# Kernel tuning notes

Measured on AMD Instinct MI355X. Metric: run time of the kernel, lower is better.

Reference implementation:

```python
import jax, jax.numpy as jnp
import numpy as np

N, DIM, H, HD, RD, QLR, OLR, G = 64, 4096, 32, 192, 64, 1536, 512, 8
BS, MAXB, L, NBLK, TOPK, EPS = 64, 64, 4096, 4096, 1024, 1e-6
SLOTS = NBLK * BS
SCALE = HD ** -0.5
NEG = -1e30


def _rms(x, w, eps=EPS):
    return x * jax.lax.rsqrt(jnp.mean(x * x, -1, keepdims=True) + eps) * w


def _rope(x, pos):
    # x: [..., RD]; pos broadcastable to x.shape[:-1]; interleaved pairs
    half = RD // 2
    inv = 1.0 / (10000.0 ** (jnp.arange(half, dtype=jnp.float32) * 2.0 / RD))
    ang = pos[..., None].astype(jnp.float32) * inv  # [..., half]
    c, s = jnp.cos(ang), jnp.sin(ang)
    xr = x.reshape(x.shape[:-1] + (half, 2))
    x0, x1 = xr[..., 0], xr[..., 1]
    return jnp.stack([x0 * c - x1 * s, x0 * s + x1 * c], -1).reshape(x.shape)


def setup_inputs() -> dict:
    key = jax.random.key(0)
    ks = jax.random.split(key, 12)
    block_tables = jax.random.permutation(ks[0], jnp.arange(N * MAXB, dtype=jnp.int32)).reshape(N, MAXB)
    context_lens = jax.random.randint(ks[1], (N,), 1, L, dtype=jnp.int32)
    last = context_lens - 1
    slot_mapping = (block_tables[jnp.arange(N), last // BS] * BS + last % BS).astype(jnp.int32)
    def w(k, shape, fan_in):
        return jax.random.normal(k, shape, jnp.float32) * (fan_in ** -0.5)
    return {
        'x': jax.random.normal(ks[2], (N, DIM), jnp.float32),
        'kv_cache': jax.random.normal(ks[3], (SLOTS, HD), jnp.float32),
        'block_tables': block_tables,
        'context_lens': context_lens,
        'slot_mapping': slot_mapping,
        'wq_a_w': w(ks[4], (QLR, DIM), DIM),
        'q_norm_w': jnp.ones((QLR,), jnp.float32),
        'wq_b_w': w(ks[5], (H * HD, QLR), QLR),
        'wkv_w': w(ks[6], (HD, DIM), DIM),
        'kv_norm_w': jnp.ones((HD,), jnp.float32),
        'wo_a_w': w(ks[7], (G, OLR, H * HD // G), H * HD // G),
        'wo_b_w': w(ks[8], (DIM, G * OLR), G * OLR),
        'attn_sink': jax.random.normal(ks[9], (H,), jnp.float32),
    }


def reference(x, kv_cache, block_tables, context_lens, slot_mapping,
              wq_a_w, q_norm_w, wq_b_w, wkv_w, kv_norm_w,
              wo_a_w, wo_b_w, attn_sink):
    pos = (context_lens - 1).astype(jnp.float32)  # [N] query positions
    # --- queries: LoRA down-proj -> RMSNorm -> up-proj -> heads ---
    q = _rms(x @ wq_a_w.T, q_norm_w) @ wq_b_w.T            # [N, H*HD]
    q = q.reshape(N, H, HD)
    q = jnp.concatenate([q[..., :HD - RD], _rope(q[..., HD - RD:], pos[:, None])], -1)
    # --- new KV latent + paged write (slot_mapping scatter) ---
    kv = _rms(x @ wkv_w.T, kv_norm_w)                       # [N, HD]
    kv = jnp.concatenate([kv[:, :HD - RD], _rope(kv[:, HD - RD:], pos)], -1)
    cache = kv_cache.at[slot_mapping].set(kv)
    # --- paged gather into dense per-request view [N, L, HD] ---
    ar = jnp.arange(L)
    slot = block_tables[:, ar // BS] * BS + ar % BS         # [N, L]
    valid = ar[None, :] < context_lens[:, None]             # [N, L]
    kv_dense = cache[jnp.where(valid, slot, 0)]
    kv_dense = jnp.where(valid[..., None], kv_dense, 0.0)
    # --- sparse top-k attention with sink logit ---
    logits = jnp.einsum('nhd,nld->nhl', q, kv_dense) * SCALE
    logits = jnp.where(valid[:, None, :], logits, NEG)
    vals, idx = jax.lax.top_k(logits, TOPK)                 # [N, H, K]
    sink = attn_sink[None, :, None]                         # [1, H, 1]
    m = jnp.maximum(jnp.max(vals, -1, keepdims=True), sink)
    e = jnp.exp(vals - m)
    denom = jnp.sum(e, -1, keepdims=True) + jnp.exp(sink - m)
    p = e / denom                                           # [N, H, K]
    probs = jnp.put_along_axis(jnp.zeros_like(logits), idx, p, axis=-1, inplace=False)
    o = jnp.einsum('nhl,nld->nhd', probs, kv_dense)         # [N, H, HD]
    # --- grouped LoRA output projection ---
    og = o.reshape(N, G, H * HD // G)
    lat = jnp.einsum('ngi,goi->ngo', og, wo_a_w).reshape(N, G * OLR)
    return lat @ wo_b_w.T                                   # [N, DIM]
```

## Files before the change

### kernel.cpp

```cpp
#include <hip/hip_runtime.h>
#include <hip/hip_bf16.h>

static constexpr float EPS_   = 1e-6f;
static constexpr float SCALE_ = 0.07216878364870323f;
static constexpr float LOG2_1E4_OVER_32 = 13.287712379549449f / 32.0f;

static constexpr long OFF_QLAT = 0;
static constexpr long OFF_Q    = OFF_QLAT + 64L * 1536;
static constexpr long OFF_KVR  = OFF_Q    + 64L * 6144;
static constexpr long OFF_O    = OFF_KVR  + 64L * 192;
static constexpr long OFF_LAT  = OFF_O    + 64L * 6144;
static constexpr long ZERO_F   = OFF_LAT  + 64L * 4096;
static constexpr long OFF_SELM = ZERO_F;
static constexpr long OFF_SELI = OFF_SELM + 2048;
static constexpr long OFF_SELT = OFF_SELI + 2048;
static constexpr long OFF_LOG  = OFF_SELT + 2048;

typedef __attribute__((ext_vector_type(8))) short bf16x8;
typedef __attribute__((ext_vector_type(4))) float f32x4;

__device__ __forceinline__ unsigned fkey(float f) {
    unsigned u = __float_as_uint(f);
    return (u & 0x80000000u) ? ~u : (u | 0x80000000u);
}
__device__ __forceinline__ float kval(unsigned k) {
    unsigned u = (k & 0x80000000u) ? (k ^ 0x80000000u) : ~k;
    return __uint_as_float(u);
}
__device__ __forceinline__ unsigned short f2bf(float f) {
    __hip_bfloat16 h = __float2bfloat16(f);
    return *reinterpret_cast<unsigned short*>(&h);
}
__device__ __forceinline__ bf16x8 pack8(float4 v0, float4 v1) {
    bf16x8 s;
    s[0] = (short)f2bf(v0.x); s[1] = (short)f2bf(v0.y);
    s[2] = (short)f2bf(v0.z); s[3] = (short)f2bf(v0.w);
    s[4] = (short)f2bf(v1.x); s[5] = (short)f2bf(v1.y);
    s[6] = (short)f2bf(v1.z); s[7] = (short)f2bf(v1.w);
    return s;
}

template <int TN>
__global__ __launch_bounds__(256) void gemm_mfma(
    const float* __restrict__ Xb, const float* __restrict__ Wb,
    float* __restrict__ Cb, int K, int ldX, int ldC, int kslice,
    long sXz, long sWz, long sCz)
{
    const float* X = Xb + (long)blockIdx.z * sXz;
    const float* W = Wb + (long)blockIdx.z * sWz;
    float*       C = Cb + (long)blockIdx.z * sCz;
    const int col0 = blockIdx.x * TN;
    const int k0   = blockIdx.y * kslice;

    __shared__ unsigned short Xs[64 * 64];
    __shared__ unsigned short Ws[TN * 64];

    const int t = threadIdx.x;
    const int w = t >> 6, lane = t & 63;
    const int m16 = lane & 15, qd = lane >> 4;
    constexpr int NT = TN / 64;

    f32x4 acc[4][NT];
#pragma unroll
    for (int mt = 0; mt < 4; ++mt)
#pragma unroll
        for (int nt = 0; nt < NT; ++nt) acc[mt][nt] = (f32x4){0.f, 0.f, 0.f, 0.f};

    for (int kt = k0; kt < k0 + kslice; kt += 64) {
#pragma unroll
        for (int i = 0; i < 2; ++i) {
            int idx = t + i * 256;
            int r = idx >> 3, u = idx & 7;
            const float* p = X + (long)r * ldX + kt + u * 8;
            float4 v0 = *(const float4*)p, v1 = *(const float4*)(p + 4);
            *(bf16x8*)(Xs + r * 64 + (u ^ (r & 7)) * 8) = pack8(v0, v1);
        }
#pragma unroll
        for (int i = 0; i < TN / 32; ++i) {
            int idx = t + i * 256;
            int r = idx >> 3, u = idx & 7;
            const float* p = W + (long)(col0 + r) * K + kt + u * 8;
            float4 v0 = *(const float4*)p, v1 = *(const float4*)(p + 4);
            *(bf16x8*)(Ws + r * 64 + (u ^ (r & 7)) * 8) = pack8(v0, v1);
        }
        __syncthreads();
#pragma unroll
        for (int ks = 0; ks < 2; ++ks) {
            int u = ks * 4 + qd;
            bf16x8 a[4], b[NT];
#pragma unroll
            for (int mt = 0; mt < 4; ++mt) {
                int row = mt * 16 + m16;
                a[mt] = *(const bf16x8*)(Xs + row * 64 + (u ^ (row & 7)) * 8);
            }
#pragma unroll
            for (int nt = 0; nt < NT; ++nt) {
                int row = (w * NT + nt) * 16 + m16;
                b[nt] = *(const bf16x8*)(Ws + row * 64 + (u ^ (row & 7)) * 8);
            }
#pragma unroll
            for (int mt = 0; mt < 4; ++mt)
#pragma unroll
                for (int nt = 0; nt < NT; ++nt)
                    acc[mt][nt] = __builtin_amdgcn_mfma_f32_16x16x32_bf16(a[mt], b[nt], acc[mt][nt], 0, 0, 0);
        }
        __syncthreads();
    }
#pragma unroll
    for (int mt = 0; mt < 4; ++mt)
#pragma unroll
        for (int nt = 0; nt < NT; ++nt) {
            int col = col0 + (w * NT + nt) * 16 + m16;
#pragma unroll
            for (int r = 0; r < 4; ++r) {
                int row = mt * 16 + qd * 4 + r;
                atomicAdd(&C[(long)row * ldC + col], acc[mt][nt][r]);
            }
        }
}

__global__ __launch_bounds__(256) void rms_rows(
    float* __restrict__ x, const float* __restrict__ w, int len)
{
    __shared__ float fred[4];
    float* row = x + (long)blockIdx.x * len;
    int t = threadIdx.x;
    float ss = 0.f;
    for (int l = t; l < len; l += 256) { float v = row[l]; ss += v * v; }
#pragma unroll
    for (int off = 32; off; off >>= 1) ss += __shfl_xor(ss, off, 64);
    if ((t & 63) == 0) fred[t >> 6] = ss;
    __syncthreads();
    ss = fred[0] + fred[1] + fred[2] + fred[3];
    float scale = rsqrtf(ss / (float)len + EPS_);
    for (int l = t; l < len; l += 256) row[l] = row[l] * scale * w[l];
}

__global__ __launch_bounds__(256) void rope_q(float* __restrict__ q,
                                              const int* __restrict__ cl)
{
    int n = blockIdx.x;
    float pos = (float)(cl[n] - 1);
    int t = threadIdx.x;
#pragma unroll
    for (int i = 0; i < 4; ++i) {
        int f = t + i * 256;
        int h = f >> 5, r = f & 31;
        float inv = exp2f(-(float)r * LOG2_1E4_OVER_32);
        float ang = pos * inv;
        float sn, cs;
        sincosf(ang, &sn, &cs);
        float* p = q + (long)n * 6144 + h * 192 + 128 + 2 * r;
        float x0 = p[0], x1 = p[1];
        p[0] = x0 * cs - x1 * sn;
        p[1] = x0 * sn + x1 * cs;
    }
}

__global__ __launch_bounds__(256) void kv_post(
    const float* __restrict__ kvr, const float* __restrict__ wnorm,
    const int* __restrict__ cl, const int* __restrict__ smap,
    float* __restrict__ kvcache)
{
    __shared__ float s[192];
    __shared__ float fred[4];
    int n = blockIdx.x, t = threadIdx.x;
    float v = (t < 192) ? kvr[(long)n * 192 + t] : 0.f;
    float ss = v * v;
#pragma unroll
    for (int off = 32; off; off >>= 1) ss += __shfl_xor(ss, off, 64);
    if ((t & 63) == 0) fred[t >> 6] = ss;
    __syncthreads();
    ss = fred[0] + fred[1] + fred[2] + fred[3];
    float scale = rsqrtf(ss / 192.f + EPS_);
    if (t < 192) s[t] = v * scale * wnorm[t];
    __syncthreads();
    if (t < 32) {
        float pos = (float)(cl[n] - 1);
        float inv = exp2f(-(float)t * LOG2_1E4_OVER_32);
        float ang = pos * inv;
        float sn, cs;
        sincosf(ang, &sn, &cs);
        float x0 = s[128 + 2 * t], x1 = s[128 + 2 * t + 1];
        s[128 + 2 * t]     = x0 * cs - x1 * sn;
        s[128 + 2 * t + 1] = x0 * sn + x1 * cs;
    }
    __syncthreads();
    if (t < 192) kvcache[(long)smap[n] * 192 + t] = s[t];
}

__global__ __launch_bounds__(256) void attn_logits_mfma(
    const float* __restrict__ q, const float* __restrict__ kvc,
    const int* __restrict__ bt, const int* __restrict__ cl,
    float* __restrict__ logits)
{
    const int n = blockIdx.y, base = blockIdx.x * 128;
    const int ctx = cl[n];
    if (base >= ctx) return;

    __shared__ unsigned short qs[32 * 192];
    __shared__ unsigned short kvs[128 * 192];
    const int t = threadIdx.x;

#pragma unroll
    for (int i = 0; i < 3; ++i) {
        int idx = t + i * 256;
        int h = idx / 24, u = idx - h * 24;
        const float* p = q + (long)n * 6144 + h * 192 + u * 8;
        float4 v0 = *(const float4*)p, v1 = *(const float4*)(p + 4);
        *(bf16x8*)(qs + h * 192 + (u ^ (h & 7)) * 8) = pack8(v0, v1);
    }
#pragma unroll
    for (int i = 0; i < 12; ++i) {
        int idx = t + i * 256;
        int l = idx / 24, u = idx - l * 24;
        int gl = min(base + l, ctx - 1);
        int slot = bt[n * 64 + (gl >> 6)] * 64 + (gl & 63);
        const float* p = kvc + (long)slot * 192 + u * 8;
        float4 v0 = *(const float4*)p, v1 = *(const float4*)(p + 4);
        *(bf16x8*)(kvs + l * 192 + (u ^ (l & 7)) * 8) = pack8(v0, v1);
    }
    __syncthreads();

    const int w = t >> 6, lane = t & 63;
    const int m16 = lane & 15, qd = lane >> 4;

    f32x4 acc[2][2];
#pragma unroll
    for (int mt = 0; mt < 2; ++mt)
#pragma unroll
        for (int nt = 0; nt < 2; ++nt) acc[mt][nt] = (f32x4){0.f, 0.f, 0.f, 0.f};

#pragma unroll
    for (int ks = 0; ks < 6; ++ks) {
        int u = ks * 4 + qd;
        bf16x8 a[2], b[2];
#pragma unroll
        for (int mt = 0; mt < 2; ++mt) {
            int row = mt * 16 + m16;
            a[mt] = *(const bf16x8*)(qs + row * 192 + (u ^ (row & 7)) * 8);
        }
#pragma unroll
        for (int nt = 0; nt < 2; ++nt) {
            int row = (2 * w + nt) * 16 + m16;
            b[nt] = *(const bf16x8*)(kvs + row * 192 + (u ^ (row & 7)) * 8);
        }
#pragma unroll
        for (int mt = 0; mt < 2; ++mt)
#pragma unroll
            for (int nt = 0; nt < 2; ++nt)
                acc[mt][nt] = __builtin_amdgcn_mfma_f32_16x16x32_bf16(a[mt], b[nt], acc[mt][nt], 0, 0, 0);
    }
#pragma unroll
    for (int mt = 0; mt < 2; ++mt)
#pragma unroll
        for (int nt = 0; nt < 2; ++nt) {
            int l = base + (2 * w + nt) * 16 + m16;
#pragma unroll
            for (int r = 0; r < 4; ++r) {
                int h = mt * 16 + qd * 4 + r;
                logits[((long)(n * 32 + h) << 12) + l] = acc[mt][nt][r] * SCALE_;
            }
        }
}

__global__ __launch_bounds__(256) void select_topk(
    const float* __restrict__ logits, const int* __restrict__ cl,
    const float* __restrict__ sink, float* __restrict__ selm,
    float* __restrict__ seli, unsigned* __restrict__ selt)
{
    int nh = blockIdx.x, n = nh >> 5, h = nh & 31;
    int ctx = cl[n];
    const float* row = logits + ((long)nh << 12);

    __shared__ unsigned keys[4096];
    __shared__ int hist[256];
    __shared__ float fred[4];
    __shared__ unsigned s_pref;
    __shared__ int s_R;

    int t = threadIdx.x;
    float mx = -3.0e38f;
    for (int l = t; l < ctx; l += 256) {
        float v = row[l];
        keys[l] = fkey(v);
        mx = fmaxf(mx, v);
    }
#pragma unroll
    for (int off = 32; off; off >>= 1) mx = fmaxf(mx, __shfl_xor(mx, off, 64));
    if ((t & 63) == 0) fred[t >> 6] = mx;
    __syncthreads();
    mx = fmaxf(fmaxf(fred[0], fred[1]), fmaxf(fred[2], fred[3]));

    unsigned tau = 0;
    if (ctx > 1024) {
        unsigned pref = 0;
        int R = 1024;
        for (int round = 3; round >= 0; --round) {
            int sh = round * 8;
            hist[t] = 0;
            __syncthreads();
            for (int l = t; l < ctx; l += 256) {
                unsigned k = keys[l];
                bool match = (round == 3) || ((k >> (sh + 8)) == (pref >> (sh + 8)));
                if (match) atomicAdd(&hist[(k >> sh) & 255], 1);
            }
            __syncthreads();
            int cum = 0;
            for (int b = t + 1; b < 256; ++b) cum += hist[b];
            if (cum < R && cum + hist[t] >= R) {
                s_pref = pref | ((unsigned)t << sh);
                s_R = R - cum;
            }
            __syncthreads();
            pref = s_pref;
            R = s_R;
            __syncthreads();
        }
        tau = pref;
    }

    float m = fmaxf(mx, sink[h]);
    float part = 0.f;
    for (int l = t; l < ctx; l += 256) {
        unsigned k = keys[l];
        if (k >= tau) part += __expf(kval(k) - m);
    }
#pragma unroll
    for (int off = 32; off; off >>= 1) part += __shfl_xor(part, off, 64);
    __syncthreads();
    if ((t & 63) == 0) fred[t >> 6] = part;
    __syncthreads();
    if (t == 0) {
        float denom = fred[0] + fred[1] + fred[2] + fred[3] + __expf(sink[h] - m);
        selm[nh] = m;
        seli[nh] = 1.0f / denom;
        selt[nh] = tau;
    }
}

__global__ __launch_bounds__(256) void attn_wsum_mfma(
    const float* __restrict__ logits, const float* __restrict__ kvc,
    const int* __restrict__ bt, const int* __restrict__ cl,
    const float* __restrict__ selm, const float* __restrict__ seli,
    const unsigned* __restrict__ selt, float* __restrict__ o)
{
    const int n = blockIdx.y, base = blockIdx.x * 128;
    const int ctx = cl[n];
    if (base >= ctx) return;
    const int vcount = min(128, ctx - base);

    __shared__ unsigned short ps[32 * 128];
    __shared__ unsigned short kvt[192 * 128];
    const int t = threadIdx.x;

#pragma unroll
    for (int i = 0; i < 2; ++i) {
        int idx = t + i * 256;
        int h = idx >> 4, u = idx & 15;
        int nh = n * 32 + h;
        float m = selm[nh], inv = seli[nh];
        unsigned tau = selt[nh];
        const float* lp = logits + ((long)nh << 12) + base + u * 8;
        float4 v0 = *(const float4*)lp, v1 = *(const float4*)(lp + 4);
        float vv[8] = {v0.x, v0.y, v0.z, v0.w, v1.x, v1.y, v1.z, v1.w};
        bf16x8 s;
#pragma unroll
        for (int j = 0; j < 8; ++j) {
            int ll = u * 8 + j;
            float p = 0.f;
            if (ll < vcount && fkey(vv[j]) >= tau) p = __expf(vv[j] - m) * inv;
            s[j] = (short)f2bf(p);
        }
        *(bf16x8*)(ps + h * 128 + (u ^ (h & 7)) * 8) = s;
    }
#pragma unroll
    for (int i = 0; i < 24; ++i) {
        int f = t + i * 256;
        int l = f & 127, d4 = f >> 7;
        int gl = min(base + l, ctx - 1);
        int slot = bt[n * 64 + (gl >> 6)] * 64 + (gl & 63);
        float4 v = *(const float4*)(kvc + (long)slot * 192 + d4 * 4);
        float vv[4] = {v.x, v.y, v.z, v.w};
#pragma unroll
        for (int e = 0; e < 4; ++e) {
            int d = d4 * 4 + e;
            int scol = (l & 7) | ((((l >> 3) ^ (d & 7)) & 15) << 3);
            kvt[d * 128 + scol] = f2bf(vv[e]);
        }
    }
    __syncthreads();

    const int w = t >> 6, lane = t & 63;
    const int m16 = lane & 15, qd = lane >> 4;

    f32x4 acc[2][3];
#pragma unroll
    for (int mt = 0; mt < 2; ++mt)
#pragma unroll
        for (int nt = 0; nt < 3; ++nt) acc[mt][nt] = (f32x4){0.f, 0.f, 0.f, 0.f};

#pragma unroll
    for (int ks = 0; ks < 4; ++ks) {
        int u = ks * 4 + qd;
        bf16x8 a[2], b[3];
#pragma unroll
        for (int mt = 0; mt < 2; ++mt) {
            int row = mt * 16 + m16;
            a[mt] = *(const bf16x8*)(ps + row * 128 + (u ^ (row & 7)) * 8);
        }
#pragma unroll
        for (int nt = 0; nt < 3; ++nt) {
            int row = (3 * w + nt) * 16 + m16;
            b[nt] = *(const bf16x8*)(kvt + row * 128 + (u ^ (row & 7)) * 8);
        }
#pragma unroll
        for (int mt = 0; mt < 2; ++mt)
#pragma unroll
            for (int nt = 0; nt < 3; ++nt)
                acc[mt][nt] = __builtin_amdgcn_mfma_f32_16x16x32_bf16(a[mt], b[nt], acc[mt][nt], 0, 0, 0);
    }
#pragma unroll
    for (int mt = 0; mt < 2; ++mt)
#pragma unroll
        for (int nt = 0; nt < 3; ++nt) {
            int d = (3 * w + nt) * 16 + m16;
#pragma unroll
            for (int r = 0; r < 4; ++r) {
                int h = mt * 16 + qd * 4 + r;
                atomicAdd(&o[(long)n * 6144 + h * 192 + d], acc[mt][nt][r]);
            }
        }
}

extern "C" void kernel_launch(void* const* d_in, const int* in_sizes, int n_in,
                              void* d_out, int out_size, void* d_ws, size_t ws_size,
                              hipStream_t stream)
{
    const float* x    = (const float*)d_in[0];
    float*       kvc  = (float*)d_in[1];
    const int*   bt   = (const int*)d_in[2];
    const int*   cl   = (const int*)d_in[3];
    const int*   smap = (const int*)d_in[4];
    const float* wqa  = (const float*)d_in[5];
    const float* qnw  = (const float*)d_in[6];
    const float* wqb  = (const float*)d_in[7];
    const float* wkv  = (const float*)d_in[8];
    const float* kvnw = (const float*)d_in[9];
    const float* woa  = (const float*)d_in[10];
    const float* wob  = (const float*)d_in[11];
    const float* sink = (const float*)d_in[12];
    float* ws  = (float*)d_ws;
    float* out = (float*)d_out;

    hipMemsetAsync(ws, 0, (size_t)ZERO_F * sizeof(float), stream);
    hipMemsetAsync(out, 0, (size_t)out_size * sizeof(float), stream);

    gemm_mfma<128><<<dim3(12, 16, 1), 256, 0, stream>>>(x, wqa, ws + OFF_QLAT,
                                                        4096, 4096, 1536, 256, 0, 0, 0);
    rms_rows<<<64, 256, 0, stream>>>(ws + OFF_QLAT, qnw, 1536);
    gemm_mfma<128><<<dim3(48, 6, 1), 256, 0, stream>>>(ws + OFF_QLAT, wqb, ws + OFF_Q,
                                                       1536, 1536, 6144, 256, 0, 0, 0);
    rope_q<<<64, 256, 0, stream>>>(ws + OFF_Q, cl);
    gemm_mfma<64><<<dim3(3, 32, 1), 256, 0, stream>>>(x, wkv, ws + OFF_KVR,
                                                      4096, 4096, 192, 128, 0, 0, 0);
    kv_post<<<64, 256, 0, stream>>>(ws + OFF_KVR, kvnw, cl, smap, kvc);
    attn_logits_mfma<<<dim3(32, 64), 256, 0, stream>>>(ws + OFF_Q, kvc, bt, cl,
                                                       ws + OFF_LOG);
    select_topk<<<2048, 256, 0, stream>>>(ws + OFF_LOG, cl, sink,
                                          ws + OFF_SELM, ws + OFF_SELI,
                                          (unsigned*)(ws + OFF_SELT));
    attn_wsum_mfma<<<dim3(32, 64), 256, 0, stream>>>(ws + OFF_LOG, kvc, bt, cl,
                                                     ws + OFF_SELM, ws + OFF_SELI,
                                                     (unsigned*)(ws + OFF_SELT),
                                                     ws + OFF_O);
    gemm_mfma<128><<<dim3(4, 3, 8), 256, 0, stream>>>(ws + OFF_O, woa, ws + OFF_LAT,
                                                      768, 6144, 4096, 256,
                                                      768, 512L * 768, 512);
    gemm_mfma<128><<<dim3(32, 8, 1), 256, 0, stream>>>(ws + OFF_LAT, wob, out,
                                                       4096, 4096, 4096, 512, 0, 0, 0);
}
```

Baseline: 541.2 us.

## Aggregate histogram atomics, scan-based radix bucket search, and two chunks per attention block

The top-k select kernel now builds its first radix histogram during the key-load pass, using wave-aggregated atomics, which removes one full pass over the keys. It also replaces the serial per-thread suffix sum over bins with a wave shuffle scan plus cross-wave sums. The logits and weighted-sum attention kernels each process two 128-token chunks per block, halving the grid. In wsum this halves the number of fp32 atomic flushes into the output and hoists the per-head selection parameters out of the loop. The trade-off is fewer blocks in flight and longer serial work per block, since each chunk is loaded behind a barrier with no overlap.

Measured after the change: 549.1 us. About the same (+1.5%).

```diff
diff --git a/kernel.cpp b/kernel.cpp
--- a/kernel.cpp
+++ b/kernel.cpp
@@ -38,6 +38,19 @@
     s[4] = (short)f2bf(v1.x); s[5] = (short)f2bf(v1.y);
     s[6] = (short)f2bf(v1.z); s[7] = (short)f2bf(v1.w);
     return s;
+}
+
+__device__ __forceinline__ void hist_add_agg(int* hist, unsigned bin, bool pred) {
+    const int lane = (int)(threadIdx.x & 63);
+    while (__any(pred)) {
+        unsigned long long act = __ballot(pred);
+        int leader = __ffsll((unsigned long long)act) - 1;
+        unsigned lbin = (unsigned)__shfl((int)bin, leader, 64);
+        bool mine = pred && (bin == lbin);
+        unsigned long long grp = __ballot(mine);
+        if (lane == leader) atomicAdd(&hist[lbin], (int)__popcll(grp));
+        if (mine) pred = false;
+    }
 }
 
 template <int TN>
@@ -194,13 +207,15 @@
     const int* __restrict__ bt, const int* __restrict__ cl,
     float* __restrict__ logits)
 {
-    const int n = blockIdx.y, base = blockIdx.x * 128;
+    const int n = blockIdx.y, sbase = blockIdx.x * 256;
     const int ctx = cl[n];
-    if (base >= ctx) return;
+    if (sbase >= ctx) return;
 
     __shared__ unsigned short qs[32 * 192];
     __shared__ unsigned short kvs[128 * 192];
     const int t = threadIdx.x;
+    const int w = t >> 6, lane = t & 63;
+    const int m16 = lane & 15, qd = lane >> 4;
 
 #pragma unroll
     for (int i = 0; i < 3; ++i) {
@@ -210,58 +225,62 @@
         float4 v0 = *(const float4*)p, v1 = *(const float4*)(p + 4);
         *(bf16x8*)(qs + h * 192 + (u ^ (h & 7)) * 8) = pack8(v0, v1);
     }
-#pragma unroll
-    for (int i = 0; i < 12; ++i) {
-        int idx = t + i * 256;
-        int l = idx / 24, u = idx - l * 24;
-        int gl = min(base + l, ctx - 1);
-        int slot = bt[n * 64 + (gl >> 6)] * 64 + (gl & 63);
-        const float* p = kvc + (long)slot * 192 + u * 8;
-        float4 v0 = *(const float4*)p, v1 = *(const float4*)(p + 4);
-        *(bf16x8*)(kvs + l * 192 + (u ^ (l & 7)) * 8) = pack8(v0, v1);
-    }
-    __syncthreads();
-
-    const int w = t >> 6, lane = t & 63;
-    const int m16 = lane & 15, qd = lane >> 4;
-
-    f32x4 acc[2][2];
-#pragma unroll
-    for (int mt = 0; mt < 2; ++mt)
-#pragma unroll
-        for (int nt = 0; nt < 2; ++nt) acc[mt][nt] = (f32x4){0.f, 0.f, 0.f, 0.f};
-
-#pragma unroll
-    for (int ks = 0; ks < 6; ++ks) {
-        int u = ks * 4 + qd;
-        bf16x8 a[2], b[2];
-#pragma unroll
-        for (int mt = 0; mt < 2; ++mt) {
-            int row = mt * 16 + m16;
-            a[mt] = *(const bf16x8*)(qs + row * 192 + (u ^ (row & 7)) * 8);
-        }
-#pragma unroll
-        for (int nt = 0; nt < 2; ++nt) {
-            int row = (2 * w + nt) * 16 + m16;
-            b[nt] = *(const bf16x8*)(kvs + row * 192 + (u ^ (row & 7)) * 8);
-        }
+
+    for (int c = 0; c < 2; ++c) {
+        const int base = sbase + c * 128;
+        if (base >= ctx) break;
+
+#pragma unroll
+        for (int i = 0; i < 12; ++i) {
+            int idx = t + i * 256;
+            int l = idx / 24, u = idx - l * 24;
+            int gl = min(base + l, ctx - 1);
+            int slot = bt[n * 64 + (gl >> 6)] * 64 + (gl & 63);
+            const float* p = kvc + (long)slot * 192 + u * 8;
+            float4 v0 = *(const float4*)p, v1 = *(const float4*)(p + 4);
+            *(bf16x8*)(kvs + l * 192 + (u ^ (l & 7)) * 8) = pack8(v0, v1);
+        }
+        __syncthreads();
+
+        f32x4 acc[2][2];
 #pragma unroll
         for (int mt = 0; mt < 2; ++mt)
 #pragma unroll
-            for (int nt = 0; nt < 2; ++nt)
-                acc[mt][nt] = __builtin_amdgcn_mfma_f32_16x16x32_bf16(a[mt], b[nt], acc[mt][nt], 0, 0, 0);
-    }
-#pragma unroll
-    for (int mt = 0; mt < 2; ++mt)
-#pragma unroll
-        for (int nt = 0; nt < 2; ++nt) {
-            int l = base + (2 * w + nt) * 16 + m16;
-#pragma unroll
-            for (int r = 0; r < 4; ++r) {
-                int h = mt * 16 + qd * 4 + r;
-                logits[((long)(n * 32 + h) << 12) + l] = acc[mt][nt][r] * SCALE_;
-            }
-        }
+            for (int nt = 0; nt < 2; ++nt) acc[mt][nt] = (f32x4){0.f, 0.f, 0.f, 0.f};
+
+#pragma unroll
+        for (int ks = 0; ks < 6; ++ks) {
+            int u = ks * 4 + qd;
+            bf16x8 a[2], b[2];
+#pragma unroll
+            for (int mt = 0; mt < 2; ++mt) {
+                int row = mt * 16 + m16;
+                a[mt] = *(const bf16x8*)(qs + row * 192 + (u ^ (row & 7)) * 8);
+            }
+#pragma unroll
+            for (int nt = 0; nt < 2; ++nt) {
+                int row = (2 * w + nt) * 16 + m16;
+                b[nt] = *(const bf16x8*)(kvs + row * 192 + (u ^ (row & 7)) * 8);
+            }
+#pragma unroll
+            for (int mt = 0; mt < 2; ++mt)
+#pragma unroll
+                for (int nt = 0; nt < 2; ++nt)
+                    acc[mt][nt] = __builtin_amdgcn_mfma_f32_16x16x32_bf16(a[mt], b[nt], acc[mt][nt], 0, 0, 0);
+        }
+#pragma unroll
+        for (int mt = 0; mt < 2; ++mt)
+#pragma unroll
+            for (int nt = 0; nt < 2; ++nt) {
+                int l = base + (2 * w + nt) * 16 + m16;
+#pragma unroll
+                for (int r = 0; r < 4; ++r) {
+                    int h = mt * 16 + qd * 4 + r;
+                    logits[((long)(n * 32 + h) << 12) + l] = acc[mt][nt][r] * SCALE_;
+                }
+            }
+        __syncthreads();
+    }
 }
 
 __global__ __launch_bounds__(256) void select_topk(
@@ -276,39 +295,70 @@
     __shared__ unsigned keys[4096];
     __shared__ int hist[256];
     __shared__ float fred[4];
+    __shared__ int wsumi[4];
     __shared__ unsigned s_pref;
     __shared__ int s_R;
 
     int t = threadIdx.x;
+    int lane = t & 63, wv = t >> 6;
+    bool need_radix = (ctx > 1024);
+
+    hist[t] = 0;
+    __syncthreads();
+
     float mx = -3.0e38f;
-    for (int l = t; l < ctx; l += 256) {
-        float v = row[l];
-        keys[l] = fkey(v);
-        mx = fmaxf(mx, v);
+    for (int l0 = 0; l0 < ctx; l0 += 256) {
+        int l = l0 + t;
+        bool valid = l < ctx;
+        unsigned k = 0;
+        if (valid) {
+            float v = row[l];
+            k = fkey(v);
+            keys[l] = k;
+            mx = fmaxf(mx, v);
+        }
+        if (need_radix) hist_add_agg(hist, k >> 24, valid);
     }
 #pragma unroll
     for (int off = 32; off; off >>= 1) mx = fmaxf(mx, __shfl_xor(mx, off, 64));
-    if ((t & 63) == 0) fred[t >> 6] = mx;
+    if (lane == 0) fred[wv] = mx;
     __syncthreads();
     mx = fmaxf(fmaxf(fred[0], fred[1]), fmaxf(fred[2], fred[3]));
 
     unsigned tau = 0;
-    if (ctx > 1024) {
+    if (need_radix) {
         unsigned pref = 0;
         int R = 1024;
         for (int round = 3; round >= 0; --round) {
             int sh = round * 8;
-            hist[t] = 0;
+            if (round < 3) {
+                hist[t] = 0;
+                __syncthreads();
+                for (int l0 = 0; l0 < ctx; l0 += 256) {
+                    int l = l0 + t;
+                    if (l < ctx) {
+                        unsigned k = keys[l];
+                        if ((k >> (sh + 8)) == (pref >> (sh + 8)))
+                            atomicAdd(&hist[(k >> sh) & 255], 1);
+                    }
+                }
+                __syncthreads();
+            }
+            int hv = hist[t];
+            int v = hv;
+#pragma unroll
+            for (int off = 1; off < 64; off <<= 1) {
+                int u2 = __shfl_down(v, off, 64);
+                if (lane + off < 64) v += u2;
+            }
+            if (lane == 0) wsumi[wv] = v;
             __syncthreads();
-            for (int l = t; l < ctx; l += 256) {
-                unsigned k = keys[l];
-                bool match = (round == 3) || ((k >> (sh + 8)) == (pref >> (sh + 8)));
-                if (match) atomicAdd(&hist[(k >> sh) & 255], 1);
-            }
-            __syncthreads();
-            int cum = 0;
-            for (int b = t + 1; b < 256; ++b) cum += hist[b];
-            if (cum < R && cum + hist[t] >= R) {
+            int above = 0;
+#pragma unroll
+            for (int w2 = 1; w2 < 4; ++w2)
+                if (wv + w2 < 4) above += wsumi[wv + w2];
+            int cum = (v - hv) + above;
+            if (cum < R && cum + hv >= R) {
                 s_pref = pref | ((unsigned)t << sh);
                 s_R = R - cum;
             }
@@ -329,7 +379,7 @@
 #pragma unroll
     for (int off = 32; off; off >>= 1) part += __shfl_xor(part, off, 64);
     __syncthreads();
-    if ((t & 63) == 0) fred[t >> 6] = part;
+    if (lane == 0) fred[wv] = part;
     __syncthreads();
     if (t == 0) {
         float denom = fred[0] + fred[1] + fred[2] + fred[3] + __expf(sink[h] - m);
@@ -345,81 +395,95 @@
     const float* __restrict__ selm, const float* __restrict__ seli,
     const unsigned* __restrict__ selt, float* __restrict__ o)
 {
-    const int n = blockIdx.y, base = blockIdx.x * 128;
+    const int n = blockIdx.y, sbase = blockIdx.x * 256;
     const int ctx = cl[n];
-    if (base >= ctx) return;
-    const int vcount = min(128, ctx - base);
+    if (sbase >= ctx) return;
 
     __shared__ unsigned short ps[32 * 128];
     __shared__ unsigned short kvt[192 * 128];
     const int t = threadIdx.x;
-
-#pragma unroll
-    for (int i = 0; i < 2; ++i) {
-        int idx = t + i * 256;
-        int h = idx >> 4, u = idx & 15;
-        int nh = n * 32 + h;
-        float m = selm[nh], inv = seli[nh];
-        unsigned tau = selt[nh];
-        const float* lp = logits + ((long)nh << 12) + base + u * 8;
-        float4 v0 = *(const float4*)lp, v1 = *(const float4*)(lp + 4);
-        float vv[8] = {v0.x, v0.y, v0.z, v0.w, v1.x, v1.y, v1.z, v1.w};
-        bf16x8 s;
-#pragma unroll
-        for (int j = 0; j < 8; ++j) {
-            int ll = u * 8 + j;
-            float p = 0.f;
-            if (ll < vcount && fkey(vv[j]) >= tau) p = __expf(vv[j] - m) * inv;
-            s[j] = (short)f2bf(p);
-        }
-        *(bf16x8*)(ps + h * 128 + (u ^ (h & 7)) * 8) = s;
-    }
-#pragma unroll
-    for (int i = 0; i < 24; ++i) {
-        int f = t + i * 256;
-        int l = f & 127, d4 = f >> 7;
-        int gl = min(base + l, ctx - 1);
-        int slot = bt[n * 64 + (gl >> 6)] * 64 + (gl & 63);
-        float4 v = *(const float4*)(kvc + (long)slot * 192 + d4 * 4);
-        float vv[4] = {v.x, v.y, v.z, v.w};
-#pragma unroll
-        for (int e = 0; e < 4; ++e) {
-            int d = d4 * 4 + e;
-            int scol = (l & 7) | ((((l >> 3) ^ (d & 7)) & 15) << 3);
-            kvt[d * 128 + scol] = f2bf(vv[e]);
-        }
-    }
-    __syncthreads();
-
     const int w = t >> 6, lane = t & 63;
     const int m16 = lane & 15, qd = lane >> 4;
 
+    float sm[2], sinv[2];
+    unsigned stau[2];
+#pragma unroll
+    for (int i = 0; i < 2; ++i) {
+        int nh = n * 32 + ((t + i * 256) >> 4);
+        sm[i] = selm[nh];
+        sinv[i] = seli[nh];
+        stau[i] = selt[nh];
+    }
+
     f32x4 acc[2][3];
 #pragma unroll
     for (int mt = 0; mt < 2; ++mt)
 #pragma unroll
         for (int nt = 0; nt < 3; ++nt) acc[mt][nt] = (f32x4){0.f, 0.f, 0.f, 0.f};
 
-#pragma unroll
-    for (int ks = 0; ks < 4; ++ks) {
-        int u = ks * 4 + qd;
-        bf16x8 a[2], b[3];
-#pragma unroll
-        for (int mt = 0; mt < 2; ++mt) {
-            int row = mt * 16 + m16;
-            a[mt] = *(const bf16x8*)(ps + row * 128 + (u ^ (row & 7)) * 8);
-        }
-#pragma unroll
-        for (int nt = 0; nt < 3; ++nt) {
-            int row = (3 * w + nt) * 16 + m16;
-            b[nt] = *(const bf16x8*)(kvt + row * 128 + (u ^ (row & 7)) * 8);
-        }
-#pragma unroll
-        for (int mt = 0; mt < 2; ++mt)
-#pragma unroll
-            for (int nt = 0; nt < 3; ++nt)
-                acc[mt][nt] = __builtin_amdgcn_mfma_f32_16x16x32_bf16(a[mt], b[nt], acc[mt][nt], 0, 0, 0);
-    }
+    for (int c = 0; c < 2; ++c) {
+        const int base = sbase + c * 128;
+        if (base >= ctx) break;
+        const int vcount = min(128, ctx - base);
+
+#pragma unroll
+        for (int i = 0; i < 2; ++i) {
+            int idx = t + i * 256;
+            int hh = idx >> 4, u = idx & 15;
+            int nh = n * 32 + hh;
+            const float* lp = logits + ((long)nh << 12) + base + u * 8;
+            float4 v0 = *(const float4*)lp, v1 = *(const float4*)(lp + 4);
+            float vv[8] = {v0.x, v0.y, v0.z, v0.w, v1.x, v1.y, v1.z, v1.w};
+            bf16x8 s;
+#pragma unroll
+            for (int j = 0; j < 8; ++j) {
+                int ll = u * 8 + j;
+                float p = 0.f;
+                if (ll < vcount && fkey(vv[j]) >= stau[i]) p = __expf(vv[j] - sm[i]) * sinv[i];
+                s[j] = (short)f2bf(p);
+            }
+            *(bf16x8*)(ps + hh * 128 + (u ^ (hh & 7)) * 8) = s;
+        }
+#pragma unroll
+        for (int i = 0; i < 24; ++i) {
+            int f = t + i * 256;
+            int l = f & 127, d4 = f >> 7;
+            int gl = min(base + l, ctx - 1);
+            int slot = bt[n * 64 + (gl >> 6)] * 64 + (gl & 63);
+            float4 v = *(const float4*)(kvc + (long)slot * 192 + d4 * 4);
+            float vv[4] = {v.x, v.y, v.z, v.w};
+#pragma unroll
+            for (int e = 0; e < 4; ++e) {
+                int d = d4 * 4 + e;
+                int scol = (l & 7) | ((((l >> 3) ^ (d & 7)) & 15) << 3);
+                kvt[d * 128 + scol] = f2bf(vv[e]);
+            }
+        }
+        __syncthreads();
+
+#pragma unroll
+        for (int ks = 0; ks < 4; ++ks) {
+            int u = ks * 4 + qd;
+            bf16x8 a[2], b[3];
+#pragma unroll
+            for (int mt = 0; mt < 2; ++mt) {
+                int row = mt * 16 + m16;
+                a[mt] = *(const bf16x8*)(ps + row * 128 + (u ^ (row & 7)) * 8);
+            }
+#pragma unroll
+            for (int nt = 0; nt < 3; ++nt) {
+                int row = (3 * w + nt) * 16 + m16;
+                b[nt] = *(const bf16x8*)(kvt + row * 128 + (u ^ (row & 7)) * 8);
+            }
+#pragma unroll
+            for (int mt = 0; mt < 2; ++mt)
+#pragma unroll
+                for (int nt = 0; nt < 3; ++nt)
+                    acc[mt][nt] = __builtin_amdgcn_mfma_f32_16x16x32_bf16(a[mt], b[nt], acc[mt][nt], 0, 0, 0);
+        }
+        __syncthreads();
+    }
+
 #pragma unroll
     for (int mt = 0; mt < 2; ++mt)
 #pragma unroll
@@ -465,12 +529,12 @@
     gemm_mfma<64><<<dim3(3, 32, 1), 256, 0, stream>>>(x, wkv, ws + OFF_KVR,
                                                       4096, 4096, 192, 128, 0, 0, 0);
     kv_post<<<64, 256, 0, stream>>>(ws + OFF_KVR, kvnw, cl, smap, kvc);
-    attn_logits_mfma<<<dim3(32, 64), 256, 0, stream>>>(ws + OFF_Q, kvc, bt, cl,
+    attn_logits_mfma<<<dim3(16, 64), 256, 0, stream>>>(ws + OFF_Q, kvc, bt, cl,
                                                        ws + OFF_LOG);
     select_topk<<<2048, 256, 0, stream>>>(ws + OFF_LOG, cl, sink,
                                           ws + OFF_SELM, ws + OFF_SELI,
                                           (unsigned*)(ws + OFF_SELT));
-    attn_wsum_mfma<<<dim3(32, 64), 256, 0, stream>>>(ws + OFF_LOG, kvc, bt, cl,
+    attn_wsum_mfma<<<dim3(16, 64), 256, 0, stream>>>(ws + OFF_LOG, kvc, bt, cl,
                                                      ws + OFF_SELM, ws + OFF_SELI,
                                                      (unsigned*)(ws + OFF_SELT),
                                                      ws + OFF_O);
```
